# Performance work log

Hardware: AMD Instinct MI355X
Metric: run time of the kernel (lower is better)

## Reference

```python
import jax, jax.numpy as jnp
import numpy as np

B, N, IN_DIM, HEADS, PER_HEAD = 8, 512, 256, 4, 32
OUT_DIM = HEADS * PER_HEAD  # 128
NEG_SLOPE = 0.2


def setup_inputs() -> dict:
    key = jax.random.key(0)
    ks = jax.random.split(key, 8)
    x = jax.random.normal(ks[0], (B, N, IN_DIM), jnp.float32)
    adj = jax.random.randint(ks[1], (B, N, N), 0, 2, jnp.int32)
    sl = 1.0 / np.sqrt(IN_DIM)
    W_l = jax.random.normal(ks[2], (IN_DIM, OUT_DIM), jnp.float32) * sl  # source proj
    b_l = jnp.zeros((OUT_DIM,), jnp.float32)
    W_r = jax.random.normal(ks[3], (IN_DIM, OUT_DIM), jnp.float32) * sl  # target proj
    b_r = jnp.zeros((OUT_DIM,), jnp.float32)
    att = jax.random.normal(ks[4], (HEADS, PER_HEAD), jnp.float32) * (1.0 / np.sqrt(PER_HEAD))
    bias = jnp.zeros((OUT_DIM,), jnp.float32)
    return {"x": x, "adj": adj, "W_l": W_l, "b_l": b_l, "W_r": W_r, "b_r": b_r,
            "att": att, "bias": bias}


def _gatv2_single(x_b, adj_b, W_l, b_l, W_r, b_r, att, bias):
    # PyG GATv2Conv: remove_self_loops + add_self_loops -> diagonal forced to 1
    n = x_b.shape[0]
    adj_sl = jnp.fill_diagonal(adj_b, 1, inplace=False)
    # edge_index = adj.nonzero().t(): source = row, target = col
    m = (adj_sl != 0).T  # m[i, j]: source j feeds target i
    xl = (x_b @ W_l + b_l).reshape(n, HEADS, PER_HEAD)  # source-side features
    xr = (x_b @ W_r + b_r).reshape(n, HEADS, PER_HEAD)  # target-side features
    s = xr[:, None] + xl[None, :]                       # [i, j, H, C]
    s = jnp.where(s > 0, s, NEG_SLOPE * s)              # LeakyReLU(0.2)
    e = jnp.einsum('ijhc,hc->ijh', s, att)              # attention logits
    e = jnp.where(m[..., None], e, -jnp.inf)
    alpha = jax.nn.softmax(e, axis=1)                   # softmax over sources j
    out = jnp.einsum('ijh,jhc->ihc', alpha, xl).reshape(n, HEADS * PER_HEAD)
    return out + bias


def reference(x, adj, W_l, b_l, W_r, b_r, att, bias):
    # Sequential per-batch processing, faithful to the original Python loop
    # and keeping the [N,N,H,C] intermediate to one graph at a time.
    def one(args):
        x_b, adj_b = args
        return _gatv2_single(x_b, adj_b, W_l, b_l, W_r, b_r, att, bias)
    return jax.lax.map(one, (x, adj))  # [B, N, OUT_DIM]
```

## Files before the change

### kernel.cpp

```cpp
#include <hip/hip_runtime.h>

#define B_   8
#define N_   512
#define IND  256
#define H_   4
#define PH   32
#define OD   128
#define TI   4

typedef float v2f __attribute__((ext_vector_type(2)));

#define ATT_SCALE 0.5770780163555854f
#define DLR_SCALE 0.8656170245333781f

template <int PAT>
__device__ __forceinline__ float dpp_add(float x) {
    int yi = __builtin_amdgcn_mov_dpp(__float_as_int(x), PAT, 0xF, 0xF, true);
    return x + __int_as_float(yi);
}

__device__ __forceinline__ float fast_exp2(float x) {
#if __has_builtin(__builtin_amdgcn_exp2f)
    return __builtin_amdgcn_exp2f(x);
#else
    return exp2f(x);
#endif
}

__device__ __forceinline__ void pk_fma(v2f& d, v2f a, v2f b) {
    asm("v_pk_fma_f32 %0, %1, %2, %0" : "+v"(d) : "v"(a), "v"(b));
}

template <int HI>
__device__ __forceinline__ void pk_fma_bc(v2f& d, v2f a, v2f b) {
    if constexpr (HI == 0)
        asm("v_pk_fma_f32 %0, %1, %2, %0 op_sel:[0,0,0] op_sel_hi:[0,1,1]"
            : "+v"(d) : "v"(a), "v"(b));
    else
        asm("v_pk_fma_f32 %0, %1, %2, %0 op_sel:[1,0,0] op_sel_hi:[1,1,1]"
            : "+v"(d) : "v"(a), "v"(b));
}

__device__ __forceinline__ v2f pk_add(v2f a, v2f b) {
    v2f d;
    asm("v_pk_add_f32 %0, %1, %2" : "=v"(d) : "v"(a), "v"(b));
    return d;
}

__global__ __launch_bounds__(512, 4) void proj_kernel(
    const float* __restrict__ x,
    const float* __restrict__ Wl, const float* __restrict__ bl,
    const float* __restrict__ Wr, const float* __restrict__ br,
    const float* __restrict__ att,
    float* __restrict__ xl, float* __restrict__ xr,
    float* __restrict__ dl, float* __restrict__ dr)
{
    __shared__ float xs[4 * IND];
    __shared__ float comb[8][64][17];

    const int t = threadIdx.x;
    const int row0 = blockIdx.x * 4;

    if (t < 256)
        ((float4*)xs)[t] = ((const float4*)(x + (size_t)row0 * IND))[t];
    __syncthreads();

    const int og    = t & 31;
    const int ks    = (t >> 5) & 7;
    const int which = t >> 8;
    const int o0 = og * 4;
    const int k0 = ks * 32;
    const float* W = (which ? Wr : Wl) + (size_t)k0 * OD + o0;

    v2f acc2[4][2];
    #pragma unroll
    for (int r = 0; r < 4; ++r) {
        acc2[r][0] = (v2f){0.f, 0.f};
        acc2[r][1] = (v2f){0.f, 0.f};
    }

    float4 wb[2][2];
    wb[0][0] = *(const float4*)(W);
    wb[0][1] = *(const float4*)(W + OD);

    #pragma unroll 2
    for (int s = 0; s < 16; ++s) {
        const int cur = s & 1, nxt = cur ^ 1;
        if (s < 15) {
            const float* Wq = W + (size_t)(2 * (s + 1)) * OD;
            wb[nxt][0] = *(const float4*)(Wq);
            wb[nxt][1] = *(const float4*)(Wq + OD);
        }
        v2f w0lo = (v2f){wb[cur][0].x, wb[cur][0].y};
        v2f w0hi = (v2f){wb[cur][0].z, wb[cur][0].w};
        v2f w1lo = (v2f){wb[cur][1].x, wb[cur][1].y};
        v2f w1hi = (v2f){wb[cur][1].z, wb[cur][1].w};
        #pragma unroll
        for (int r = 0; r < 4; ++r) {
            float2 xv = *(const float2*)(&xs[r * IND + k0 + 2 * s]);
            v2f xp = (v2f){xv.x, xv.y};
            pk_fma_bc<0>(acc2[r][0], xp, w0lo);
            pk_fma_bc<0>(acc2[r][1], xp, w0hi);
            pk_fma_bc<1>(acc2[r][0], xp, w1lo);
            pk_fma_bc<1>(acc2[r][1], xp, w1hi);
        }
    }

    const int pid = og | (which << 5);
    #pragma unroll
    for (int r = 0; r < 4; ++r) {
        comb[ks][pid][r * 4 + 0] = acc2[r][0].x;
        comb[ks][pid][r * 4 + 1] = acc2[r][0].y;
        comb[ks][pid][r * 4 + 2] = acc2[r][1].x;
        comb[ks][pid][r * 4 + 3] = acc2[r][1].y;
    }
    __syncthreads();

    const int cf  = t & 63;
    const int rf  = (t >> 6) & 3;
    const int whf = t >> 8;
    const int pidf = (cf >> 1) | (whf << 5);
    const int ci   = (cf & 1) * 2;
    const float* bb = whf ? br : bl;
    float* dst = whf ? xr : xl;
    float* dp  = whf ? dr : dl;
    float2 bv = *(const float2*)(bb + cf * 2);
    float2 av = *(const float2*)(att + cf * 2);
    float y[2];
    #pragma unroll
    for (int c = 0; c < 2; ++c) {
        const int idx = rf * 4 + ci + c;
        float s01 = comb[0][pidf][idx] + comb[1][pidf][idx];
        float s23 = comb[2][pidf][idx] + comb[3][pidf][idx];
        float s45 = comb[4][pidf][idx] + comb[5][pidf][idx];
        float s67 = comb[6][pidf][idx] + comb[7][pidf][idx];
        y[c] = ((s01 + s23) + (s45 + s67)) + ((c == 0) ? bv.x : bv.y);
    }
    *(float2*)(&dst[(size_t)(row0 + rf) * OD + cf * 2]) =
        make_float2(y[0], y[1]);
    float dc = fmaf(av.x, y[0], av.y * y[1]);
    dc += __shfl_xor(dc, 1);
    dc += __shfl_xor(dc, 2);
    dc += __shfl_xor(dc, 4);
    dc += __shfl_xor(dc, 8);
    if ((cf & 15) == 0)
        dp[(size_t)(row0 + rf) * H_ + (cf >> 4)] = DLR_SCALE * dc;
}

__global__ __launch_bounds__(512, 4) void attn_kernel(
    const int* __restrict__ adj, const float* __restrict__ att,
    const float* __restrict__ bias,
    const float* __restrict__ xl, const float* __restrict__ xr,
    const float* __restrict__ dl, const float* __restrict__ dr,
    float* __restrict__ out)
{
    __shared__ float sacc[H_][2][32][PH + 1];
    __shared__ float ssum[H_][32][TI];

    const int t = threadIdx.x;
    const int bid = (blockIdx.x & 7) * 128 + (blockIdx.x >> 3);
    const int b  = bid >> 7;
    const int i0 = (bid & 127) * TI;
    const int cq = t & 3;
    const int js = (t >> 2) & 31;
    const int h  = t >> 7;
    const int cbase = h * PH + cq * 8;

    float atS[8];
    {
        const float* ap = att + cbase;
        float4 a0 = *(const float4*)(ap);
        float4 a1 = *(const float4*)(ap + 4);
        atS[0] = ATT_SCALE * a0.x; atS[1] = ATT_SCALE * a0.y;
        atS[2] = ATT_SCALE * a0.z; atS[3] = ATT_SCALE * a0.w;
        atS[4] = ATT_SCALE * a1.x; atS[5] = ATT_SCALE * a1.y;
        atS[6] = ATT_SCALE * a1.z; atS[7] = ATT_SCALE * a1.w;
    }
    v2f xrv[TI][4];
    #pragma unroll
    for (int il = 0; il < TI; ++il) {
        const float* xp = xr + ((size_t)(b * N_ + i0 + il)) * OD + cbase;
        float4 r0 = *(const float4*)(xp);
        float4 r1 = *(const float4*)(xp + 4);
        xrv[il][0] = (v2f){r0.x, r0.y};
        xrv[il][1] = (v2f){r0.z, r0.w};
        xrv[il][2] = (v2f){r1.x, r1.y};
        xrv[il][3] = (v2f){r1.z, r1.w};
    }

    v2f acc[TI][4];
    float sumw[TI];
    #pragma unroll
    for (int il = 0; il < TI; ++il) {
        sumw[il] = 0.f;
        #pragma unroll
        for (int m = 0; m < 4; ++m) acc[il][m] = (v2f){0.f, 0.f};
    }

    const float* xlp = xl + ((size_t)(b * N_ + js)) * OD + cbase;
    const int*   ajp = adj + ((size_t)(b * N_ + js)) * N_ + i0;
    const float* dlp = dl + ((size_t)(b * N_ + js)) * H_ + h;

    float4 va = *(const float4*)(xlp);
    float4 vb = *(const float4*)(xlp + 4);
    int4   mj = *(const int4*)(ajp);
    float  dj = *dlp;

    #pragma unroll 2
    for (int u = 0; u < 16; ++u) {
        float4 wa = va, wb = vb;
        int4   wm = mj;
        float  wd = dj;
        if (u < 15) {
            xlp += 32 * OD; ajp += 32 * N_; dlp += 32 * H_;
            va = *(const float4*)(xlp);
            vb = *(const float4*)(xlp + 4);
            mj = *(const int4*)(ajp);
            dj = *dlp;
        }
        const int j = u * 32 + js;
        v2f p0 = (v2f){wa.x, wa.y}, p1 = (v2f){wa.z, wa.w};
        v2f p2 = (v2f){wb.x, wb.y}, p3 = (v2f){wb.z, wb.w};
        int wmv[TI] = {wm.x, wm.y, wm.z, wm.w};
        #pragma unroll
        for (int il = 0; il < TI; ++il) {
            v2f s01 = pk_add(xrv[il][0], p0);
            v2f s23 = pk_add(xrv[il][1], p1);
            v2f s45 = pk_add(xrv[il][2], p2);
            v2f s67 = pk_add(xrv[il][3], p3);
            float e2a = 0.f, e2b = 0.f;
            e2a = fmaf(atS[0], __builtin_fabsf(s01.x), e2a);
            e2b = fmaf(atS[1], __builtin_fabsf(s01.y), e2b);
            e2a = fmaf(atS[2], __builtin_fabsf(s23.x), e2a);
            e2b = fmaf(atS[3], __builtin_fabsf(s23.y), e2b);
            e2a = fmaf(atS[4], __builtin_fabsf(s45.x), e2a);
            e2b = fmaf(atS[5], __builtin_fabsf(s45.y), e2b);
            e2a = fmaf(atS[6], __builtin_fabsf(s67.x), e2a);
            e2b = fmaf(atS[7], __builtin_fabsf(s67.y), e2b);
            float eh = e2a + e2b;
            eh = dpp_add<0xB1>(eh);
            eh = dpp_add<0x4E>(eh);
            float e = wd + eh;
            bool keep = (wmv[il] != 0) || (j == i0 + il);
            float w = keep ? fast_exp2(e) : 0.f;
            sumw[il] += w;
            v2f ws = (v2f){w, w};
            pk_fma(acc[il][0], ws, p0);
            pk_fma(acc[il][1], ws, p1);
            pk_fma(acc[il][2], ws, p2);
            pk_fma(acc[il][3], ws, p3);
        }
    }

    if (cq == 0) {
        #pragma unroll
        for (int il = 0; il < TI; ++il)
            ssum[h][js][il] = sumw[il];
    }
    #pragma unroll
    for (int p = 0; p < 2; ++p) {
        *(float4*)(&sacc[h][p][js][cq * 8]) =
            make_float4(acc[p][0].x, acc[p][0].y, acc[p][1].x, acc[p][1].y);
        *(float4*)(&sacc[h][p][js][cq * 8 + 4]) =
            make_float4(acc[p][2].x, acc[p][2].y, acc[p][3].x, acc[p][3].y);
    }
    __syncthreads();
    if (t < 256) {
        const int c   = t & 31;
        const int ilr = (t >> 5) & 1;
        const int hr  = t >> 6;
        float a = 0.f, st = 0.f;
        #pragma unroll
        for (int k = 0; k < 32; ++k) {
            a  += sacc[hr][ilr][k][c];
            st += ssum[hr][k][ilr];
        }
        const int cg = hr * PH + c;
        out[((size_t)(b * N_ + i0 + ilr)) * OD + cg] =
            fmaf(a, 1.f / st, bias[cg]);
    }
    __syncthreads();
    #pragma unroll
    for (int p = 0; p < 2; ++p) {
        *(float4*)(&sacc[h][p][js][cq * 8]) =
            make_float4(acc[2 + p][0].x, acc[2 + p][0].y,
                        acc[2 + p][1].x, acc[2 + p][1].y);
        *(float4*)(&sacc[h][p][js][cq * 8 + 4]) =
            make_float4(acc[2 + p][2].x, acc[2 + p][2].y,
                        acc[2 + p][3].x, acc[2 + p][3].y);
    }
    __syncthreads();
    if (t < 256) {
        const int c   = t & 31;
        const int ilr = (t >> 5) & 1;
        const int hr  = t >> 6;
        float a = 0.f, st = 0.f;
        #pragma unroll
        for (int k = 0; k < 32; ++k) {
            a  += sacc[hr][ilr][k][c];
            st += ssum[hr][k][2 + ilr];
        }
        const int cg = hr * PH + c;
        out[((size_t)(b * N_ + i0 + 2 + ilr)) * OD + cg] =
            fmaf(a, 1.f / st, bias[cg]);
    }
}

extern "C" void kernel_launch(void* const* d_in, const int* in_sizes, int n_in,
                              void* d_out, int out_size, void* d_ws, size_t ws_size,
                              hipStream_t stream) {
    const float* x    = (const float*)d_in[0];
    const int*   adj  = (const int*)d_in[1];
    const float* Wl   = (const float*)d_in[2];
    const float* bl   = (const float*)d_in[3];
    const float* Wr   = (const float*)d_in[4];
    const float* br   = (const float*)d_in[5];
    const float* att  = (const float*)d_in[6];
    const float* bias = (const float*)d_in[7];
    float* out = (float*)d_out;

    float* xl = (float*)d_ws;
    float* xr = xl + (size_t)B_ * N_ * OD;
    float* dl = xr + (size_t)B_ * N_ * OD;
    float* dr = dl + (size_t)B_ * N_ * H_;

    proj_kernel<<<1024, 512, 0, stream>>>(x, Wl, bl, Wr, br, att, xl, xr, dl, dr);
    attn_kernel<<<1024, 512, 0, stream>>>(adj, att, bias, xl, xr, dl, dr, out);
}
```

Measured before the change: 121.7 us.

## Precompute additive float edge mask in projection kernel, double rows per projection block

The projection kernel now handles 8 rows per block (512 blocks) and also turns the int adjacency, with the self-loop diagonal folded in, into an additive float mask (0 or -1e30) in workspace. The attention kernel adds this mask to the logit and always takes exp2, which removes the per-edge compare and select. The cost is an extra 8 MB write plus a read of the same 8 MB, which adds global memory traffic. Doubling rows per block reuses each weight load over more rows but raises register pressure, so the occupancy hint drops to 2.

```diff
diff --git a/kernel.cpp b/kernel.cpp
--- a/kernel.cpp
+++ b/kernel.cpp
@@ -47,22 +47,22 @@
     return d;
 }
 
-__global__ __launch_bounds__(512, 4) void proj_kernel(
-    const float* __restrict__ x,
+__global__ __launch_bounds__(512, 2) void proj_kernel(
+    const float* __restrict__ x, const int* __restrict__ adj,
     const float* __restrict__ Wl, const float* __restrict__ bl,
     const float* __restrict__ Wr, const float* __restrict__ br,
     const float* __restrict__ att,
     float* __restrict__ xl, float* __restrict__ xr,
-    float* __restrict__ dl, float* __restrict__ dr)
+    float* __restrict__ dl, float* __restrict__ dr,
+    float* __restrict__ emask)
 {
-    __shared__ float xs[4 * IND];
-    __shared__ float comb[8][64][17];
+    __shared__ float xs[8 * IND];
+    __shared__ float comb[8][64][33];
 
     const int t = threadIdx.x;
-    const int row0 = blockIdx.x * 4;
-
-    if (t < 256)
-        ((float4*)xs)[t] = ((const float4*)(x + (size_t)row0 * IND))[t];
+    const int row0 = blockIdx.x * 8;
+
+    ((float4*)xs)[t] = ((const float4*)(x + (size_t)row0 * IND))[t];
     __syncthreads();
 
     const int og    = t & 31;
@@ -72,9 +72,9 @@
     const int k0 = ks * 32;
     const float* W = (which ? Wr : Wl) + (size_t)k0 * OD + o0;
 
-    v2f acc2[4][2];
-    #pragma unroll
-    for (int r = 0; r < 4; ++r) {
+    v2f acc2[8][2];
+    #pragma unroll
+    for (int r = 0; r < 8; ++r) {
         acc2[r][0] = (v2f){0.f, 0.f};
         acc2[r][1] = (v2f){0.f, 0.f};
     }
@@ -96,7 +96,7 @@
         v2f w1lo = (v2f){wb[cur][1].x, wb[cur][1].y};
         v2f w1hi = (v2f){wb[cur][1].z, wb[cur][1].w};
         #pragma unroll
-        for (int r = 0; r < 4; ++r) {
+        for (int r = 0; r < 8; ++r) {
             float2 xv = *(const float2*)(&xs[r * IND + k0 + 2 * s]);
             v2f xp = (v2f){xv.x, xv.y};
             pk_fma_bc<0>(acc2[r][0], xp, w0lo);
@@ -108,7 +108,7 @@
 
     const int pid = og | (which << 5);
     #pragma unroll
-    for (int r = 0; r < 4; ++r) {
+    for (int r = 0; r < 8; ++r) {
         comb[ks][pid][r * 4 + 0] = acc2[r][0].x;
         comb[ks][pid][r * 4 + 1] = acc2[r][0].y;
         comb[ks][pid][r * 4 + 2] = acc2[r][1].x;
@@ -116,39 +116,57 @@
     }
     __syncthreads();
 
-    const int cf  = t & 63;
-    const int rf  = (t >> 6) & 3;
+    const int ogf = t & 31;
+    const int rf  = (t >> 5) & 7;
     const int whf = t >> 8;
-    const int pidf = (cf >> 1) | (whf << 5);
-    const int ci   = (cf & 1) * 2;
+    const int pidf = ogf | (whf << 5);
     const float* bb = whf ? br : bl;
     float* dst = whf ? xr : xl;
     float* dp  = whf ? dr : dl;
-    float2 bv = *(const float2*)(bb + cf * 2);
-    float2 av = *(const float2*)(att + cf * 2);
-    float y[2];
-    #pragma unroll
-    for (int c = 0; c < 2; ++c) {
-        const int idx = rf * 4 + ci + c;
+    float4 bv = *(const float4*)(bb + ogf * 4);
+    float4 av = *(const float4*)(att + ogf * 4);
+    const float bvf[4] = {bv.x, bv.y, bv.z, bv.w};
+    const float avf[4] = {av.x, av.y, av.z, av.w};
+    float y[4];
+    #pragma unroll
+    for (int c = 0; c < 4; ++c) {
+        const int idx = rf * 4 + c;
         float s01 = comb[0][pidf][idx] + comb[1][pidf][idx];
         float s23 = comb[2][pidf][idx] + comb[3][pidf][idx];
         float s45 = comb[4][pidf][idx] + comb[5][pidf][idx];
         float s67 = comb[6][pidf][idx] + comb[7][pidf][idx];
-        y[c] = ((s01 + s23) + (s45 + s67)) + ((c == 0) ? bv.x : bv.y);
-    }
-    *(float2*)(&dst[(size_t)(row0 + rf) * OD + cf * 2]) =
-        make_float2(y[0], y[1]);
-    float dc = fmaf(av.x, y[0], av.y * y[1]);
+        y[c] = ((s01 + s23) + (s45 + s67)) + bvf[c];
+    }
+    *(float4*)(&dst[(size_t)(row0 + rf) * OD + ogf * 4]) =
+        make_float4(y[0], y[1], y[2], y[3]);
+    float dc = fmaf(avf[0], y[0], fmaf(avf[1], y[1],
+               fmaf(avf[2], y[2], avf[3] * y[3])));
     dc += __shfl_xor(dc, 1);
     dc += __shfl_xor(dc, 2);
     dc += __shfl_xor(dc, 4);
-    dc += __shfl_xor(dc, 8);
-    if ((cf & 15) == 0)
-        dp[(size_t)(row0 + rf) * H_ + (cf >> 4)] = DLR_SCALE * dc;
+    if ((ogf & 7) == 0)
+        dp[(size_t)(row0 + rf) * H_ + (ogf >> 3)] = DLR_SCALE * dc;
+
+    const int base = blockIdx.x * 512 + t;
+    #pragma unroll
+    for (int kq = 0; kq < 2; ++kq) {
+        const int q = base + kq * 262144;
+        const int i0q = (q & 127) * 4;
+        const int jq  = (q >> 7) & 511;
+        const int bq  = q >> 16;
+        const size_t off = ((size_t)(bq * N_ + jq)) * N_ + i0q;
+        int4 a4 = *(const int4*)(adj + off);
+        float4 m;
+        m.x = (a4.x != 0 || i0q + 0 == jq) ? 0.f : -1e30f;
+        m.y = (a4.y != 0 || i0q + 1 == jq) ? 0.f : -1e30f;
+        m.z = (a4.z != 0 || i0q + 2 == jq) ? 0.f : -1e30f;
+        m.w = (a4.w != 0 || i0q + 3 == jq) ? 0.f : -1e30f;
+        *(float4*)(emask + off) = m;
+    }
 }
 
 __global__ __launch_bounds__(512, 4) void attn_kernel(
-    const int* __restrict__ adj, const float* __restrict__ att,
+    const float* __restrict__ emask, const float* __restrict__ att,
     const float* __restrict__ bias,
     const float* __restrict__ xl, const float* __restrict__ xr,
     const float* __restrict__ dl, const float* __restrict__ dr,
@@ -198,30 +216,29 @@
     }
 
     const float* xlp = xl + ((size_t)(b * N_ + js)) * OD + cbase;
-    const int*   ajp = adj + ((size_t)(b * N_ + js)) * N_ + i0;
+    const float* emp = emask + ((size_t)(b * N_ + js)) * N_ + i0;
     const float* dlp = dl + ((size_t)(b * N_ + js)) * H_ + h;
 
     float4 va = *(const float4*)(xlp);
     float4 vb = *(const float4*)(xlp + 4);
-    int4   mj = *(const int4*)(ajp);
+    float4 mj = *(const float4*)(emp);
     float  dj = *dlp;
 
     #pragma unroll 2
     for (int u = 0; u < 16; ++u) {
         float4 wa = va, wb = vb;
-        int4   wm = mj;
+        float4 wm = mj;
         float  wd = dj;
         if (u < 15) {
-            xlp += 32 * OD; ajp += 32 * N_; dlp += 32 * H_;
+            xlp += 32 * OD; emp += 32 * N_; dlp += 32 * H_;
             va = *(const float4*)(xlp);
             vb = *(const float4*)(xlp + 4);
-            mj = *(const int4*)(ajp);
+            mj = *(const float4*)(emp);
             dj = *dlp;
         }
-        const int j = u * 32 + js;
         v2f p0 = (v2f){wa.x, wa.y}, p1 = (v2f){wa.z, wa.w};
         v2f p2 = (v2f){wb.x, wb.y}, p3 = (v2f){wb.z, wb.w};
-        int wmv[TI] = {wm.x, wm.y, wm.z, wm.w};
+        float wmv[TI] = {wm.x, wm.y, wm.z, wm.w};
         #pragma unroll
         for (int il = 0; il < TI; ++il) {
             v2f s01 = pk_add(xrv[il][0], p0);
@@ -240,9 +257,8 @@
             float eh = e2a + e2b;
             eh = dpp_add<0xB1>(eh);
             eh = dpp_add<0x4E>(eh);
-            float e = wd + eh;
-            bool keep = (wmv[il] != 0) || (j == i0 + il);
-            float w = keep ? fast_exp2(e) : 0.f;
+            float e = (wd + wmv[il]) + eh;
+            float w = fast_exp2(e);
             sumw[il] += w;
             v2f ws = (v2f){w, w};
             pk_fma(acc[il][0], ws, p0);
@@ -319,11 +335,13 @@
     const float* bias = (const float*)d_in[7];
     float* out = (float*)d_out;
 
-    float* xl = (float*)d_ws;
-    float* xr = xl + (size_t)B_ * N_ * OD;
-    float* dl = xr + (size_t)B_ * N_ * OD;
-    float* dr = dl + (size_t)B_ * N_ * H_;
-
-    proj_kernel<<<1024, 512, 0, stream>>>(x, Wl, bl, Wr, br, att, xl, xr, dl, dr);
-    attn_kernel<<<1024, 512, 0, stream>>>(adj, att, bias, xl, xr, dl, dr, out);
-}
+    float* xl    = (float*)d_ws;
+    float* xr    = xl + (size_t)B_ * N_ * OD;
+    float* dl    = xr + (size_t)B_ * N_ * OD;
+    float* dr    = dl + (size_t)B_ * N_ * H_;
+    float* emask = dr + (size_t)B_ * N_ * H_;
+
+    proj_kernel<<<512, 512, 0, stream>>>(x, adj, Wl, bl, Wr, br, att,
+                                         xl, xr, dl, dr, emask);
+    attn_kernel<<<1024, 512, 0, stream>>>(emask, att, bias, xl, xr, dl, dr, out);
+}
```

New measurement: 125.2 us. 2.9% more time.
